# Optimization experiments

Measured on AMD Instinct MI355X. Metric: run time of the kernel, lower is better.

## Reference

```python
import jax, jax.numpy as jnp
import numpy as np

E = 1_000_000   # num_embeddings
D = 128         # embedding_dim
C = 262_144     # cuda_row_num (cache slots)
N = 16_384      # ids per step


def setup_inputs() -> dict:
    key = jax.random.key(0)
    k1, k2, k3 = jax.random.split(key, 3)
    ids = jax.random.randint(k1, (N,), 0, E, dtype=jnp.int64)
    weight = jax.random.normal(k2, (E, D), dtype=jnp.float32)       # CPU-side full table
    cuda_weight = weight[:C]                                          # warmed-up cache: slot s holds row s
    freq_cnter = jax.random.randint(k3, (E,), 0, 100, dtype=jnp.int64)
    idx_map = jnp.arange(E, dtype=jnp.int64)                          # identity (no dataset reorder)
    cached_idx_map = jnp.arange(C, dtype=jnp.int64)                   # slot -> cached row id (full cache)
    inverted_cached_idx = jnp.where(jnp.arange(E) < C, jnp.arange(E), -1).astype(jnp.int64)
    return {"ids": ids, "idx_map": idx_map, "cached_idx_map": cached_idx_map,
            "inverted_cached_idx": inverted_cached_idx, "freq_cnter": freq_cnter,
            "weight": weight, "cuda_weight": cuda_weight}


def reference(ids, idx_map, cached_idx_map, inverted_cached_idx, freq_cnter, weight, cuda_weight):
    """Faithful functional prepare_ids: unique -> miss detect -> LFU evict ->
    write-back evicted rows to CPU weight -> load missed rows into cache ->
    index translation. Static shapes: unique padded to N with sentinel E;
    OOB scatter indices (== E or == C) are dropped."""
    rows = idx_map[ids]                                   # [N] cpu row ids
    u = jnp.unique(rows, size=N, fill_value=E)            # [N] padded unique
    valid = u < E
    u_safe = jnp.where(valid, u, 0)
    slot_of_u = jnp.where(valid, inverted_cached_idx[u_safe], -1)
    hit = valid & (slot_of_u >= 0)
    miss = valid & (slot_of_u < 0)                        # rows needing CPU->GPU transfer

    # -- LFU eviction: protect slots holding rows in the current backlist (u) --
    protected = jnp.zeros((C,), bool).at[jnp.where(hit, slot_of_u, C)].set(True, mode='drop')
    cached_rows = cached_idx_map                          # [C], -1 == empty slot
    keys = freq_cnter[jnp.clip(cached_rows, 0, E - 1)]
    keys = jnp.where(cached_rows < 0, jnp.int64(-1), keys)            # empty slots used first
    keys = jnp.where(protected, jnp.iinfo(keys.dtype).max, keys)      # never evict backlist
    order = jnp.argsort(keys)                             # slots in eviction priority

    rank = jnp.cumsum(miss) - 1                           # position among misses
    slot_for = jnp.where(miss, order[jnp.clip(rank, 0, C - 1)], C)    # C == dropped
    slot_for_safe = jnp.clip(slot_for, 0, C - 1)
    evicted_rows = cached_rows[slot_for_safe]

    # write-back evicted rows to CPU weight (skip empty slots)
    wb_row = jnp.where(miss & (evicted_rows >= 0), evicted_rows, E)
    weight_new = weight.at[wb_row].set(cuda_weight[slot_for_safe], mode='drop')
    # load missed rows into freed cache slots
    cuda_new = cuda_weight.at[slot_for].set(weight_new[u_safe], mode='drop')

    # update index maps
    inv = inverted_cached_idx.at[wb_row].set(-1, mode='drop')
    inv = inv.at[jnp.where(miss, u, E)].set(slot_for, mode='drop')
    cached_new = cached_idx_map.at[slot_for].set(jnp.where(miss, u, -1), mode='drop')

    gpu_row_idxs = inv[rows]                              # [N] cache slot per input id
    freq_new = freq_cnter.at[jnp.where(valid, u, E)].add(1, mode='drop')
    out = cuda_new[gpu_row_idxs]                          # [N, D] gathered embeddings
    return gpu_row_idxs, out
```

## Files before the change

kernel.cpp:

```cpp
#include <hip/hip_runtime.h>

#define E_TOT 1000000
#define D_DIM 128
#define C_CAP 262144
#define N_IDS 16384
#define NB 102
#define NW 31250
#define SB 256
#define NTHR 512
#define SPB 1024
#define MWB 62
#define CHK 52

static_assert(SB * SPB == C_CAP, "geometry");
static_assert(MWB * NTHR >= NW, "geometry");
static_assert(5 * CHK >= SB, "geometry");
static_assert(5 * NB <= NTHR, "geometry");

__device__ __forceinline__ int cnt_eq(unsigned w, unsigned pat) {
    unsigned x = w ^ pat;
    unsigned y = ((x & 0x7F7F7F7Fu) + 0x7F7F7F7Fu) | x | 0x7F7F7F7Fu;
    return __popc(~y & 0x80808080u);
}

__device__ __forceinline__ int bucket_of(int crow, const int* __restrict__ freq) {
    int key = (crow < 0) ? -1 : freq[crow < E_TOT ? crow : (E_TOT - 1)];
    return (key < 0) ? 0 : (key >= 100 ? 101 : key + 1);
}

__device__ __forceinline__ int block_exscan(int v, int tid, int* lds8) {
    int lane = tid & 63, wv = tid >> 6;
    int incl = v;
#pragma unroll
    for (int o = 1; o < 64; o <<= 1) {
        int u = __shfl_up(incl, o, 64);
        if (lane >= o) incl += u;
    }
    if (lane == 63) lds8[wv] = incl;
    __syncthreads();
    int wsum = 0;
    for (int w = 0; w < wv; ++w) wsum += lds8[w];
    __syncthreads();
    return wsum + incl - v;
}

__global__ __launch_bounds__(256) void scatter_k(
    const int* __restrict__ ids, const int* __restrict__ idx_map,
    const int* __restrict__ inv, unsigned* __restrict__ protBits,
    unsigned* __restrict__ missBits) {
    int i = blockIdx.x * 256 + threadIdx.x;
    int id = ids[i];
    if (id < 0 || id >= E_TOT) return;
    int row = idx_map[id];
    if (row < 0 || row >= E_TOT) return;
    int s = inv[row];
    if (s >= 0) {
        if (s < C_CAP) atomicOr(&protBits[s >> 5], 1u << (s & 31));
    } else {
        atomicOr(&missBits[row >> 5], 1u << (row & 31));
    }
}

__global__ __launch_bounds__(NTHR) void count_k(
    const unsigned* __restrict__ protBits, const int* __restrict__ cidx,
    const int* __restrict__ freq, const unsigned* __restrict__ missBits,
    unsigned short* __restrict__ bucketArr2, int* __restrict__ blockHist,
    int* __restrict__ wordPrefix, int* __restrict__ blockSumMiss) {
    __shared__ int waveHist[8][NB];
    __shared__ int lds8[8];
    const int tid = threadIdx.x, bid = blockIdx.x;
    if (bid < SB) {
        for (int k = tid; k < 8 * NB; k += NTHR) ((int*)waveHist)[k] = 0;
        __syncthreads();
        const int s0 = bid * SPB + 2 * tid;
        const int2 cr = *(const int2*)(cidx + s0);
        const unsigned pw = protBits[s0 >> 5];
        int b0 = ((pw >> (s0 & 31)) & 1u) ? 255 : bucket_of(cr.x, freq);
        int b1 = ((pw >> ((s0 & 31) + 1)) & 1u) ? 255 : bucket_of(cr.y, freq);
        const int wv = tid >> 6;
        if (b0 != 255) atomicAdd(&waveHist[wv][b0], 1);
        if (b1 != 255) atomicAdd(&waveHist[wv][b1], 1);
        bucketArr2[bid * (SPB / 2) + tid] = (unsigned short)(b0 | (b1 << 8));
        __syncthreads();
        if (tid < NB) {
            int s = 0;
#pragma unroll
            for (int w = 0; w < 8; ++w) s += waveHist[w][tid];
            blockHist[bid * NB + tid] = s;
        }
    } else {
        const int j = bid - SB;
        const int w = j * NTHR + tid;
        int v = (w < NW) ? __popc(missBits[w]) : 0;
        int excl = block_exscan(v, tid, lds8);
        if (w < NW) wordPrefix[w] = excl;
        if (tid == NTHR - 1) blockSumMiss[j] = excl + v;
    }
}

__global__ __launch_bounds__(NTHR) void place_k(
    const unsigned short* __restrict__ bucketArr2,
    const int* __restrict__ blockHist, const int* __restrict__ blockSumMiss,
    int* __restrict__ wordPrefix, int* __restrict__ order) {
    const int tid = threadIdx.x, bid = blockIdx.x;
    if (bid < SB) {
        __shared__ unsigned char ldsB[SPB];
        __shared__ int waveHist[8][NB];
        __shared__ int partBefore[5][NB];
        __shared__ int partTotal[5][NB];
        __shared__ int bstart[NB];
        __shared__ int before[NB];
        __shared__ int mTot;
        ((unsigned short*)ldsB)[tid] = bucketArr2[bid * (SPB / 2) + tid];
        for (int k = tid; k < 8 * NB; k += NTHR) ((int*)waveHist)[k] = 0;
        __syncthreads();
        const int b0 = ldsB[2 * tid], b1 = ldsB[2 * tid + 1];
        const int wv = tid >> 6, lane = tid & 63;
        if (b0 != 255) atomicAdd(&waveHist[wv][b0], 1);
        if (b1 != 255) atomicAdd(&waveHist[wv][b1], 1);
        if (tid < 5 * NB) {
            const int c = tid / NB, b = tid % NB;
            int lo = c * CHK, hi = lo + CHK;
            if (hi > SB) hi = SB;
            int tot = 0, bef = 0;
            for (int blk = lo; blk < hi; ++blk) {
                int v = blockHist[blk * NB + b];
                tot += v;
                if (blk < bid) bef += v;
            }
            partTotal[c][b] = tot;
            partBefore[c][b] = bef;
        }
        __syncthreads();
        if (tid < NB) {
            int t = 0, bf = 0;
#pragma unroll
            for (int c = 0; c < 5; ++c) {
                t += partTotal[c][tid];
                bf += partBefore[c][tid];
            }
            bstart[tid] = t;
            before[tid] = bf;
        }
        __syncthreads();
        if (tid == 0) {
            int run = 0;
            for (int b = 0; b < NB; ++b) {
                int t = bstart[b];
                bstart[b] = run;
                run += t;
            }
        } else if (tid == 64) {
            int m = 0;
            for (int k = 0; k < MWB; ++k) m += blockSumMiss[k];
            mTot = m;
        }
        __syncthreads();
        const int m = mTot;
        const unsigned* wp = (const unsigned*)&ldsB[wv * 128];
        unsigned patA = 0x01010101u * (unsigned)b0;
        unsigned patB = 0x01010101u * (unsigned)b1;
        int full = lane >> 1;
        int cA = 0, cB = 0;
        for (int w = 0; w < full; ++w) {
            unsigned x = wp[w];
            cA += cnt_eq(x, patA);
            cB += cnt_eq(x, patB);
        }
        if (lane & 1) {
            unsigned x = wp[full] | 0xFFFF0000u;
            cA += cnt_eq(x, patA);
            cB += cnt_eq(x, patB);
        }
        int pA = 0, pB = 0;
        for (int w = 0; w < wv; ++w) {
            pA += (b0 != 255) ? waveHist[w][b0] : 0;
            pB += (b1 != 255) ? waveHist[w][b1] : 0;
        }
        const int s0 = bid * SPB + 2 * tid;
        if (b0 != 255) {
            int pos = bstart[b0] + before[b0] + pA + cA;
            if (pos < m) order[pos] = s0;
        }
        if (b1 != 255) {
            int pos = bstart[b1] + before[b1] + pB + cB + ((b0 == b1) ? 1 : 0);
            if (pos < m) order[pos] = s0 + 1;
        }
    } else {
        const int j = bid - SB;
        int add = 0;
        for (int k = 0; k < j; ++k) add += blockSumMiss[k];
        const int w = j * NTHR + tid;
        if (w < NW) wordPrefix[w] += add;
    }
}

__global__ __launch_bounds__(NTHR) void final_k(
    const int* __restrict__ ids, const int* __restrict__ idx_map,
    const int* __restrict__ inv, const unsigned* __restrict__ missBits,
    const int* __restrict__ wordPrefix, const int* __restrict__ order,
    const float* __restrict__ weight, const float* __restrict__ cuda_weight,
    float* __restrict__ out) {
    const int i = blockIdx.x * 8 + (threadIdx.x >> 6);
    const int lane = threadIdx.x & 63;
    int id = ids[i];
    int row = (id >= 0 && id < E_TOT) ? idx_map[id] : 0;
    row = row < 0 ? 0 : (row >= E_TOT ? E_TOT - 1 : row);
    int s0 = inv[row];
    int slot;
    const float* src;
    if (s0 >= 0) {
        slot = s0;
        src = cuda_weight + (size_t)slot * D_DIM;
    } else {
        int w = row >> 5;
        unsigned mask = (1u << (row & 31)) - 1u;
        int rank = wordPrefix[w] + __popc(missBits[w] & mask);
        rank = rank < 0 ? 0 : (rank >= N_IDS ? N_IDS - 1 : rank);
        slot = order[rank];
        src = weight + (size_t)row * D_DIM;
    }
    if (lane == 0) out[i] = (float)slot;
    const float2* s2 = (const float2*)src;
    float2* d2 = (float2*)(out + N_IDS + (size_t)i * D_DIM);
    d2[lane] = s2[lane];
}

extern "C" void kernel_launch(void* const* d_in, const int* in_sizes, int n_in,
                              void* d_out, int out_size, void* d_ws, size_t ws_size,
                              hipStream_t stream) {
    const int* ids     = (const int*)d_in[0];
    const int* idx_map = (const int*)d_in[1];
    const int* cidx    = (const int*)d_in[2];
    const int* inv     = (const int*)d_in[3];
    const int* freq    = (const int*)d_in[4];
    const float* weight      = (const float*)d_in[5];
    const float* cuda_weight = (const float*)d_in[6];
    float* out = (float*)d_out;

    unsigned char* ws = (unsigned char*)d_ws;
    size_t o = 0;
    auto take = [&](size_t bytes) {
        size_t r = o;
        o += (bytes + 255) & ~(size_t)255;
        return r;
    };
    unsigned* protBits = (unsigned*)(ws + take(C_CAP / 8));
    unsigned* missBits = (unsigned*)(ws + take((size_t)NW * 4));
    size_t zbytes = o;
    unsigned short* bucketArr2 = (unsigned short*)(ws + take(C_CAP));
    int* blockHist    = (int*)(ws + take((size_t)SB * NB * 4));
    int* wordPrefix   = (int*)(ws + take((size_t)NW * 4));
    int* blockSumMiss = (int*)(ws + take(MWB * 4));
    int* order        = (int*)(ws + take((size_t)N_IDS * 4));
    (void)ws_size; (void)in_sizes; (void)n_in; (void)out_size;

    hipMemsetAsync(ws, 0, zbytes, stream);

    scatter_k<<<N_IDS / 256, 256, 0, stream>>>(ids, idx_map, inv, protBits,
                                               missBits);

    count_k<<<SB + MWB, NTHR, 0, stream>>>(protBits, cidx, freq, missBits,
                                           bucketArr2, blockHist, wordPrefix,
                                           blockSumMiss);

    place_k<<<SB + MWB, NTHR, 0, stream>>>(bucketArr2, blockHist, blockSumMiss,
                                           wordPrefix, order);

    final_k<<<N_IDS / 8, NTHR, 0, stream>>>(ids, idx_map, inv, missBits,
                                            wordPrefix, order, weight,
                                            cuda_weight, out);
}
```

Before: 35.21 us.

## Merge scatter into bucket counting and compute protection via atomic decrements

Fuses the id-scatter kernel into the bucket-histogram kernel. Protected slots are removed from the histograms with atomic decrements instead of being masked before counting, and block, super-block and total histograms are built with global atomics. The miss-word prefix scan moves into a single block of the placement kernel, and placement uses super-block partial sums instead of chunked scans, cutting one launch. In exchange the order array is written for all unprotected slots (up to C entries) rather than just the first m, which adds global writes and extra atomic contention.

```diff
diff --git a/kernel.cpp b/kernel.cpp
--- a/kernel.cpp
+++ b/kernel.cpp
@@ -9,13 +9,10 @@
 #define SB 256
 #define NTHR 512
 #define SPB 1024
-#define MWB 62
-#define CHK 52
+#define NSUP 16
 
 static_assert(SB * SPB == C_CAP, "geometry");
-static_assert(MWB * NTHR >= NW, "geometry");
-static_assert(5 * CHK >= SB, "geometry");
-static_assert(5 * NB <= NTHR, "geometry");
+static_assert(SB / NSUP == 16, "geometry");
 
 __device__ __forceinline__ int cnt_eq(unsigned w, unsigned pat) {
     unsigned x = w ^ pat;
@@ -44,103 +41,96 @@
     return wsum + incl - v;
 }
 
-__global__ __launch_bounds__(256) void scatter_k(
+__global__ __launch_bounds__(NTHR) void combo1_k(
     const int* __restrict__ ids, const int* __restrict__ idx_map,
-    const int* __restrict__ inv, unsigned* __restrict__ protBits,
-    unsigned* __restrict__ missBits) {
-    int i = blockIdx.x * 256 + threadIdx.x;
-    int id = ids[i];
-    if (id < 0 || id >= E_TOT) return;
-    int row = idx_map[id];
-    if (row < 0 || row >= E_TOT) return;
-    int s = inv[row];
-    if (s >= 0) {
-        if (s < C_CAP) atomicOr(&protBits[s >> 5], 1u << (s & 31));
-    } else {
-        atomicOr(&missBits[row >> 5], 1u << (row & 31));
-    }
-}
-
-__global__ __launch_bounds__(NTHR) void count_k(
-    const unsigned* __restrict__ protBits, const int* __restrict__ cidx,
-    const int* __restrict__ freq, const unsigned* __restrict__ missBits,
-    unsigned short* __restrict__ bucketArr2, int* __restrict__ blockHist,
-    int* __restrict__ wordPrefix, int* __restrict__ blockSumMiss) {
-    __shared__ int waveHist[8][NB];
-    __shared__ int lds8[8];
+    const int* __restrict__ inv, const int* __restrict__ cidx,
+    const int* __restrict__ freq,
+    unsigned* __restrict__ protBits, unsigned* __restrict__ missBits,
+    unsigned short* __restrict__ bucketArr2,
+    int* __restrict__ blockHist, int* __restrict__ superHist,
+    int* __restrict__ bucketTotal) {
     const int tid = threadIdx.x, bid = blockIdx.x;
     if (bid < SB) {
+        __shared__ int waveHist[8][NB];
         for (int k = tid; k < 8 * NB; k += NTHR) ((int*)waveHist)[k] = 0;
         __syncthreads();
         const int s0 = bid * SPB + 2 * tid;
         const int2 cr = *(const int2*)(cidx + s0);
-        const unsigned pw = protBits[s0 >> 5];
-        int b0 = ((pw >> (s0 & 31)) & 1u) ? 255 : bucket_of(cr.x, freq);
-        int b1 = ((pw >> ((s0 & 31) + 1)) & 1u) ? 255 : bucket_of(cr.y, freq);
+        const int b0 = bucket_of(cr.x, freq);
+        const int b1 = bucket_of(cr.y, freq);
         const int wv = tid >> 6;
-        if (b0 != 255) atomicAdd(&waveHist[wv][b0], 1);
-        if (b1 != 255) atomicAdd(&waveHist[wv][b1], 1);
+        atomicAdd(&waveHist[wv][b0], 1);
+        atomicAdd(&waveHist[wv][b1], 1);
         bucketArr2[bid * (SPB / 2) + tid] = (unsigned short)(b0 | (b1 << 8));
         __syncthreads();
         if (tid < NB) {
             int s = 0;
 #pragma unroll
             for (int w = 0; w < 8; ++w) s += waveHist[w][tid];
-            blockHist[bid * NB + tid] = s;
+            if (s) {
+                atomicAdd(&blockHist[bid * NB + tid], s);
+                atomicAdd(&superHist[(bid >> 4) * NB + tid], s);
+                atomicAdd(&bucketTotal[tid], s);
+            }
         }
     } else {
-        const int j = bid - SB;
-        const int w = j * NTHR + tid;
-        int v = (w < NW) ? __popc(missBits[w]) : 0;
-        int excl = block_exscan(v, tid, lds8);
-        if (w < NW) wordPrefix[w] = excl;
-        if (tid == NTHR - 1) blockSumMiss[j] = excl + v;
-    }
-}
-
-__global__ __launch_bounds__(NTHR) void place_k(
+        const int i = (bid - SB) * NTHR + tid;
+        int id = ids[i];
+        if (id < 0 || id >= E_TOT) return;
+        int row = idx_map[id];
+        if (row < 0 || row >= E_TOT) return;
+        int s = inv[row];
+        if (s >= 0) {
+            if (s < C_CAP) {
+                unsigned bit = 1u << (s & 31);
+                unsigned old = atomicOr(&protBits[s >> 5], bit);
+                if (!(old & bit)) {
+                    int b = bucket_of(cidx[s], freq);
+                    atomicAdd(&blockHist[(s >> 10) * NB + b], -1);
+                    atomicAdd(&superHist[(s >> 14) * NB + b], -1);
+                    atomicAdd(&bucketTotal[b], -1);
+                }
+            }
+        } else {
+            atomicOr(&missBits[row >> 5], 1u << (row & 31));
+        }
+    }
+}
+
+__global__ __launch_bounds__(NTHR) void combo2_k(
     const unsigned short* __restrict__ bucketArr2,
-    const int* __restrict__ blockHist, const int* __restrict__ blockSumMiss,
+    const unsigned* __restrict__ protBits,
+    const int* __restrict__ blockHist, const int* __restrict__ superHist,
+    const int* __restrict__ bucketTotal, const unsigned* __restrict__ missBits,
     int* __restrict__ wordPrefix, int* __restrict__ order) {
     const int tid = threadIdx.x, bid = blockIdx.x;
     if (bid < SB) {
         __shared__ unsigned char ldsB[SPB];
+        __shared__ unsigned protW[SPB / 32];
         __shared__ int waveHist[8][NB];
-        __shared__ int partBefore[5][NB];
-        __shared__ int partTotal[5][NB];
+        __shared__ int before[NB];
         __shared__ int bstart[NB];
-        __shared__ int before[NB];
-        __shared__ int mTot;
-        ((unsigned short*)ldsB)[tid] = bucketArr2[bid * (SPB / 2) + tid];
+        if (tid < SPB / 32) protW[tid] = protBits[bid * (SPB / 32) + tid];
         for (int k = tid; k < 8 * NB; k += NTHR) ((int*)waveHist)[k] = 0;
         __syncthreads();
-        const int b0 = ldsB[2 * tid], b1 = ldsB[2 * tid + 1];
+        const unsigned short pk = bucketArr2[bid * (SPB / 2) + tid];
+        const unsigned pw = protW[tid >> 4];
+        int b0 = ((pw >> ((2 * tid) & 31)) & 1u) ? 255 : (pk & 0xFF);
+        int b1 = ((pw >> ((2 * tid + 1) & 31)) & 1u) ? 255 : (pk >> 8);
+        ldsB[2 * tid] = (unsigned char)b0;
+        ldsB[2 * tid + 1] = (unsigned char)b1;
         const int wv = tid >> 6, lane = tid & 63;
         if (b0 != 255) atomicAdd(&waveHist[wv][b0], 1);
         if (b1 != 255) atomicAdd(&waveHist[wv][b1], 1);
-        if (tid < 5 * NB) {
-            const int c = tid / NB, b = tid % NB;
-            int lo = c * CHK, hi = lo + CHK;
-            if (hi > SB) hi = SB;
-            int tot = 0, bef = 0;
-            for (int blk = lo; blk < hi; ++blk) {
-                int v = blockHist[blk * NB + b];
-                tot += v;
-                if (blk < bid) bef += v;
-            }
-            partTotal[c][b] = tot;
-            partBefore[c][b] = bef;
-        }
         __syncthreads();
         if (tid < NB) {
-            int t = 0, bf = 0;
-#pragma unroll
-            for (int c = 0; c < 5; ++c) {
-                t += partTotal[c][tid];
-                bf += partBefore[c][tid];
-            }
-            bstart[tid] = t;
-            before[tid] = bf;
+            const int S = bid >> 4;
+            int bef = 0;
+            for (int sp = 0; sp < S; ++sp) bef += superHist[sp * NB + tid];
+            for (int blk = S * 16; blk < bid; ++blk)
+                bef += blockHist[blk * NB + tid];
+            before[tid] = bef;
+            bstart[tid] = bucketTotal[tid];
         }
         __syncthreads();
         if (tid == 0) {
@@ -150,13 +140,8 @@
                 bstart[b] = run;
                 run += t;
             }
-        } else if (tid == 64) {
-            int m = 0;
-            for (int k = 0; k < MWB; ++k) m += blockSumMiss[k];
-            mTot = m;
-        }
-        __syncthreads();
-        const int m = mTot;
+        }
+        __syncthreads();
         const unsigned* wp = (const unsigned*)&ldsB[wv * 128];
         unsigned patA = 0x01010101u * (unsigned)b0;
         unsigned patB = 0x01010101u * (unsigned)b1;
@@ -178,20 +163,28 @@
             pB += (b1 != 255) ? waveHist[w][b1] : 0;
         }
         const int s0 = bid * SPB + 2 * tid;
-        if (b0 != 255) {
-            int pos = bstart[b0] + before[b0] + pA + cA;
-            if (pos < m) order[pos] = s0;
-        }
-        if (b1 != 255) {
-            int pos = bstart[b1] + before[b1] + pB + cB + ((b0 == b1) ? 1 : 0);
-            if (pos < m) order[pos] = s0 + 1;
-        }
+        if (b0 != 255)
+            order[bstart[b0] + before[b0] + pA + cA] = s0;
+        if (b1 != 255)
+            order[bstart[b1] + before[b1] + pB + cB + ((b0 == b1) ? 1 : 0)] =
+                s0 + 1;
     } else {
-        const int j = bid - SB;
-        int add = 0;
-        for (int k = 0; k < j; ++k) add += blockSumMiss[k];
-        const int w = j * NTHR + tid;
-        if (w < NW) wordPrefix[w] += add;
+        __shared__ int lds8[8];
+        const int WPT = (NW + NTHR - 1) / NTHR;
+        const int w0 = tid * WPT;
+        int sum = 0;
+        for (int k = 0; k < WPT; ++k) {
+            int w = w0 + k;
+            if (w < NW) sum += __popc(missBits[w]);
+        }
+        int run = block_exscan(sum, tid, lds8);
+        for (int k = 0; k < WPT; ++k) {
+            int w = w0 + k;
+            if (w < NW) {
+                wordPrefix[w] = run;
+                run += __popc(missBits[w]);
+            }
+        }
     }
 }
 
@@ -216,7 +209,7 @@
         int w = row >> 5;
         unsigned mask = (1u << (row & 31)) - 1u;
         int rank = wordPrefix[w] + __popc(missBits[w] & mask);
-        rank = rank < 0 ? 0 : (rank >= N_IDS ? N_IDS - 1 : rank);
+        rank = rank < 0 ? 0 : (rank >= C_CAP ? C_CAP - 1 : rank);
         slot = order[rank];
         src = weight + (size_t)row * D_DIM;
     }
@@ -247,25 +240,24 @@
     };
     unsigned* protBits = (unsigned*)(ws + take(C_CAP / 8));
     unsigned* missBits = (unsigned*)(ws + take((size_t)NW * 4));
+    int* blockHist   = (int*)(ws + take((size_t)SB * NB * 4));
+    int* superHist   = (int*)(ws + take((size_t)NSUP * NB * 4));
+    int* bucketTotal = (int*)(ws + take(NB * 4));
     size_t zbytes = o;
     unsigned short* bucketArr2 = (unsigned short*)(ws + take(C_CAP));
-    int* blockHist    = (int*)(ws + take((size_t)SB * NB * 4));
-    int* wordPrefix   = (int*)(ws + take((size_t)NW * 4));
-    int* blockSumMiss = (int*)(ws + take(MWB * 4));
-    int* order        = (int*)(ws + take((size_t)N_IDS * 4));
+    int* wordPrefix = (int*)(ws + take((size_t)NW * 4));
+    int* order      = (int*)(ws + take((size_t)C_CAP * 4));
     (void)ws_size; (void)in_sizes; (void)n_in; (void)out_size;
 
     hipMemsetAsync(ws, 0, zbytes, stream);
 
-    scatter_k<<<N_IDS / 256, 256, 0, stream>>>(ids, idx_map, inv, protBits,
-                                               missBits);
-
-    count_k<<<SB + MWB, NTHR, 0, stream>>>(protBits, cidx, freq, missBits,
-                                           bucketArr2, blockHist, wordPrefix,
-                                           blockSumMiss);
-
-    place_k<<<SB + MWB, NTHR, 0, stream>>>(bucketArr2, blockHist, blockSumMiss,
-                                           wordPrefix, order);
+    combo1_k<<<SB + N_IDS / NTHR, NTHR, 0, stream>>>(
+        ids, idx_map, inv, cidx, freq, protBits, missBits, bucketArr2,
+        blockHist, superHist, bucketTotal);
+
+    combo2_k<<<SB + 1, NTHR, 0, stream>>>(bucketArr2, protBits, blockHist,
+                                          superHist, bucketTotal, missBits,
+                                          wordPrefix, order);
 
     final_k<<<N_IDS / 8, NTHR, 0, stream>>>(ids, idx_map, inv, missBits,
                                             wordPrefix, order, weight,
```

Result: slower. 83.41 us (+136.9%).
